# Kernel optimization log

Hardware: AMD Instinct MI355X
Metric: run time of the kernel (lower is better)

The kernel has to match this reference:

```python
import jax, jax.numpy as jnp
import numpy as np

B, N, F, L = 16, 1536, 128, 2   # batch, input_features, enc(=dec)_features, n_layers
SLOPE = 0.2                      # LeakyReLU alpha
NEG = -1e9                       # mask fill for softmax


def setup_inputs() -> dict:
    key = jax.random.key(0)
    ks = jax.random.split(key, 14)
    g = lambda k, shape, s=0.05: (jax.random.normal(k, shape, jnp.float32) * s)
    data = jax.random.randint(ks[0], (B, N), 0, 2)          # binary presence vector
    embed = g(ks[1], (N + 1, F)).at[0].set(0.0)              # padding_idx=0 row zeroed
    return {
        "data": data,
        "embed": embed,
        "enc_W": g(ks[2], (L, F, F)),
        "enc_a_src": g(ks[3], (L, F)),
        "enc_a_dst": g(ks[4], (L, F)),
        "param_W": g(ks[5], (F, 2 * F)),
        "param_b": g(ks[6], (2 * F,)),
        "dec_W": g(ks[7], (F, F)),
        "dec_a_src": g(ks[8], (F,)),
        "dec_a_dst": g(ks[9], (F,)),
        "out_W1": g(ks[10], (F, F)),
        "out_b1": g(ks[11], (F,)),
        "out_W2": g(ks[12], (F, 1)),
        "out_b2": g(ks[13], (1,)),
    }


def _gat(x, mask, W, a_src, a_dst):
    """Single-head graph attention over a dense boolean adjacency `mask`.
    Equivalent to sparse GAT over the clique edge list data_to_edges() builds
    (self-loops included). Rows with no edges output 0."""
    h = x @ W                                    # (n, F)
    si = h @ a_src                               # (n,)
    sj = h @ a_dst                               # (n,)
    e = jax.nn.leaky_relu(si[:, None] + sj[None, :], SLOPE)
    e = jnp.where(mask, e, NEG)
    attn = jax.nn.softmax(e, axis=-1) * mask.any(axis=-1)[:, None]
    return attn @ h                              # (n, F)


def reference(data, embed, enc_W, enc_a_src, enc_a_dst, param_W, param_b,
              dec_W, dec_a_src, dec_a_dst, out_W1, out_b1, out_W2, out_b2):
    def per_sample(g):
        d = g != 0                               # active feature nodes
        m_in = d[:, None] & d[None, :]           # input clique adjacency (N, N)
        x = embed[:-1]                           # node features = embedding rows (N, F)
        for l in range(L):                       # encoder layers (n_layers=2)
            x = jax.nn.elu(_gat(x, m_in, enc_W[l], enc_a_src[l], enc_a_dst[l]))
        # variational parameterization (eval mode: dropout=id, reparam -> mean)
        par = x @ param_W + param_b              # (N, 2F)
        mean, sigma = par[:, :F], par[:, F:]
        w = (g == 1).astype(mean.dtype)
        cnt = jnp.maximum(w.sum(), 1.0)
        kld = 0.5 * jnp.sum(w[:, None] * (jnp.exp(sigma) - sigma - 1.0 + mean ** 2)) / cnt
        # append master node (last embedding row) and decode over extended clique
        enc_full = jnp.concatenate([mean, embed[-1:]], axis=0)      # (N+1, F)
        d_ext = jnp.concatenate([d, jnp.ones((1,), bool)])
        m_out = d_ext[:, None] & d_ext[None, :]                     # (N+1, N+1)
        dec = jax.nn.relu(_gat(enc_full, m_out, dec_W, dec_a_src, dec_a_dst))
        return dec[-1], kld                      # master-node readout (F,)

    feats, klds = jax.vmap(per_sample)(data)     # (B, F), (B,)
    pred = jax.nn.relu(feats @ out_W1 + out_b1) @ out_W2 + out_b2   # (B, 1)
    return pred, jnp.sum(klds)
```

## Files before the change

### kernel.cpp

```cpp
#include <hip/hip_runtime.h>

#define BB 16
#define NN 1536
#define FF 128
#define SLOPE 0.2f
#define NS 2048
#define CH2 32
#define NCH2 48
#define TI 8
#define NPB (NN/8)
#define DCS 64
#define NDC 24

__global__ __launch_bounds__(1024) void k_sortpre(
    const int* __restrict__ data,
    const float* __restrict__ embed, const float* __restrict__ decW,
    const float* __restrict__ aS, const float* __restrict__ aD,
    const float* __restrict__ SJb, long sStride,
    int* __restrict__ actG, int* __restrict__ cntG,
    float* __restrict__ hN, float* __restrict__ sN,
    float* __restrict__ keyG, int* __restrict__ pjG,
    float* __restrict__ SBG, float* __restrict__ SDG)
{
  int b = blockIdx.x, t = threadIdx.x;
  if (b == BB){
    __shared__ float rs[2][2];
    if (t < FF){
      float acc = 0.f;
      for (int k=0;k<FF;++k) acc += embed[(long)NN*FF + k] * decW[k*FF + t];
      hN[t] = acc;
      float ps = acc * aS[t];
      float pd = acc * aD[t];
      #pragma unroll
      for (int o=32;o;o>>=1){ ps += __shfl_down(ps,o); pd += __shfl_down(pd,o); }
      if ((t&63)==0){ rs[0][t>>6]=ps; rs[1][t>>6]=pd; }
    }
    __syncthreads();
    if (t==0){ sN[0]=rs[0][0]+rs[0][1]; sN[1]=rs[1][0]+rs[1][1]; }
    return;
  }

  __shared__ float key[NS]; __shared__ int pj[NS];
  __shared__ float sb[NS]; __shared__ float sd[NS];
  __shared__ int cntS;
  int cnt;
  if (data != nullptr){
    __shared__ int s[256];
    const int PER = NN/256;
    int local[NN/256]; int nl = 0;
    if (t < 256){
      int base = t*PER;
      #pragma unroll
      for (int u=0; u<PER; ++u){
        if (data[b*NN + base + u] != 0) local[nl++] = base+u;
      }
      s[t]=nl;
    }
    __syncthreads();
    if (t==0){ int run=0; for (int i=0;i<256;i++){ int v=s[i]; s[i]=run; run+=v; }
               cntG[b]=run; cntS=run; }
    __syncthreads();
    if (t < 256){
      int o = s[t];
      for (int u=0; u<nl; ++u) actG[b*NN + o + u] = local[u];
    }
    __syncthreads();
    cnt = cntS;
  } else {
    cnt = cntG[b];
  }

  const float* SJ = SJb + (long)b*sStride;
  const int* act = (data != nullptr) ? actG + b*NN : nullptr;
  int NSort = 32; while (NSort < cnt) NSort <<= 1;

  for (int e=t; e<NSort; e+=1024){
    if (e<cnt){ int io = act ? act[e] : e; key[e]=SJ[io]; pj[e]=io; }
    else { key[e]=__builtin_inff(); pj[e]=0; }
  }
  __syncthreads();

  for (int k=2; k<=NSort; k<<=1){
    for (int j=k>>1; j>=64; j>>=1){
      for (int e=t; e<NSort; e+=1024){
        int l = e ^ j;
        if (l > e){
          bool asc = ((e & k) == 0);
          float a0=key[e], a1=key[l];
          if (asc ? (a0>a1) : (a0<a1)){
            key[e]=a1; key[l]=a0; int p=pj[e]; pj[e]=pj[l]; pj[l]=p;
          }
        }
      }
      __syncthreads();
    }
    {
      float v0=0.f, v1=0.f; int q0=0, q1=0;
      if (t < NSort){ v0=key[t]; q0=pj[t]; }
      if (NSort > 1024){ v1=key[t+1024]; q1=pj[t+1024]; }
      int jstart = ((k>>1) < 32) ? (k>>1) : 32;
      for (int j=jstart; j>0; j>>=1){
        {
          float ov=__shfl_xor(v0,j); int oq=__shfl_xor(q0,j);
          bool keepmin = (((t & k)==0) == ((t & j)==0));
          bool take = keepmin ? (ov < v0) : (ov > v0);
          if (take){ v0=ov; q0=oq; }
        }
        if (NSort > 1024){
          int e = t+1024;
          float ov=__shfl_xor(v1,j); int oq=__shfl_xor(q1,j);
          bool keepmin = (((e & k)==0) == ((e & j)==0));
          bool take = keepmin ? (ov < v1) : (ov > v1);
          if (take){ v1=ov; q1=oq; }
        }
      }
      if (t < NSort){ key[t]=v0; pj[t]=q0; }
      if (NSort > 1024){ key[t+1024]=v1; pj[t+1024]=q1; }
    }
    __syncthreads();
  }

  {
    int e0 = 2*t, e1 = 2*t+1;
    float b0=0.f,b1=0.f,d0=0.f,d1=0.f;
    if (e0 < cnt){ float kk=key[e0]; b0=__expf(kk); d0=__expf(SLOPE*kk); }
    if (e1 < cnt){ float kk=key[e1]; b1=__expf(kk); d1=__expf(SLOPE*kk); }
    float sB=b0+b1, sD=d0+d1;
    int lane = t & 63, wid = t >> 6;
    float iB=sB, iD=sD;
    #pragma unroll
    for (int o=1;o<64;o<<=1){
      float uB=__shfl_up(iB,o), uD=__shfl_up(iD,o);
      if (lane>=o){ iB+=uB; iD+=uD; }
    }
    __shared__ float wsB[16], wsD[16];
    if (lane==63){ wsB[wid]=iB; wsD[wid]=iD; }
    __syncthreads();
    float offB=0.f, offD=0.f;
    for (int w=0; w<wid; ++w){ offB+=wsB[w]; offD+=wsD[w]; }
    float exB = offB + iB - sB;
    float exD = offD + iD - sD;
    if (e0 < NSort){ sb[e0]=exB+b0;    sd[e0]=exD+d0; }
    if (e1 < NSort){ sb[e1]=exB+b0+b1; sd[e1]=exD+d0+d1; }
  }
  __syncthreads();

  for (int e=t; e<cnt; e+=1024){
    keyG[(long)b*NN+e]=key[e]; pjG[(long)b*NN+e]=pj[e];
    SBG[(long)b*NN+e]=sb[e];   SDG[(long)b*NN+e]=sd[e];
  }
}

__global__ __launch_bounds__(128) void k_rowmm(const float* __restrict__ Xv,
    const float* __restrict__ W, const float* __restrict__ aS, const float* __restrict__ aD,
    float* __restrict__ H, float* __restrict__ SI, float* __restrict__ SJ)
{
  int r0 = blockIdx.x*8;
  int f = threadIdx.x;
  __shared__ float xs[8][FF];
  #pragma unroll
  for (int r=0;r<8;++r) xs[r][f] = Xv[(long)(r0+r)*FF + f];
  __syncthreads();
  float acc[8]={0.f,0.f,0.f,0.f,0.f,0.f,0.f,0.f};
  for (int k=0;k<FF;++k){
    float w = W[k*FF + f];
    #pragma unroll
    for (int r=0;r<8;++r) acc[r] += xs[r][k]*w;
  }
  float as = aS[f], ad = aD[f];
  __shared__ float red[2][8][2];
  #pragma unroll
  for (int r=0;r<8;++r){
    H[(long)(r0+r)*FF + f] = acc[r];
    float ps = acc[r]*as, pd = acc[r]*ad;
    #pragma unroll
    for (int o=32;o;o>>=1){ ps += __shfl_down(ps,o); pd += __shfl_down(pd,o); }
    if ((f&63)==0){ red[0][r][f>>6]=ps; red[1][r][f>>6]=pd; }
  }
  __syncthreads();
  if (f<8){
    SI[r0+f]=red[0][f][0]+red[0][f][1]; SJ[r0+f]=red[1][f][0]+red[1][f][1];
  }
}

__global__ __launch_bounds__(128) void k_chunk(
    const float* __restrict__ keyG, const int* __restrict__ pjG,
    const int* __restrict__ cntArr,
    const float* __restrict__ Hb, long hStride,
    float* __restrict__ PP, float* __restrict__ PM)
{
  int b = blockIdx.y, c = blockIdx.x, f = threadIdx.x;
  int cnt = cntArr[b];
  int k0 = c*CH2;
  if (k0 >= cnt) return;
  int k1 = k0+CH2; if (k1 > cnt) k1 = cnt;
  int kn = k1-k0;
  const float* H = Hb + (long)b*hStride + f;
  __shared__ int pjs[CH2]; __shared__ float wbs[CH2], wds[CH2];
  if (f < CH2 && f < kn){
    float kk = keyG[(long)b*NN + k0 + f];
    pjs[f] = pjG[(long)b*NN + k0 + f];
    wbs[f] = __expf(kk);
    wds[f] = __expf(SLOPE*kk);
  }
  __syncthreads();
  float accB=0.f, accD=0.f;
  float hbuf[8];
  #pragma unroll
  for (int i=0;i<8;i++) hbuf[i] = (i<kn) ? H[(long)pjs[i]*FF] : 0.f;
  long obase = ((long)b*NN + k0)*FF + f;
  int k=0;
  for (; k+8<=kn; k+=8){
    #pragma unroll
    for (int u=0;u<8;u++){
      float hv = hbuf[u];
      int kp = k+u+8;
      hbuf[u] = (kp<kn) ? H[(long)pjs[kp]*FF] : 0.f;
      accB = fmaf(wbs[k+u], hv, accB);
      accD = fmaf(wds[k+u], hv, accD);
      PP[obase + (long)(k+u)*FF] = accB;
      PM[obase + (long)(k+u)*FF] = accD;
    }
  }
  for (; k<kn; ++k){
    float hv = H[(long)pjs[k]*FF];
    accB = fmaf(wbs[k], hv, accB);
    accD = fmaf(wds[k], hv, accD);
    PP[obase + (long)k*FF] = accB;
    PM[obase + (long)k*FF] = accD;
  }
}

__global__ __launch_bounds__(128) void k_offs(
    const float* __restrict__ PP, const float* __restrict__ PM,
    const int* __restrict__ cntArr,
    float* __restrict__ OFB, float* __restrict__ OFD)
{
  int b = blockIdx.x, f = threadIdx.x;
  int cnt = cntArr[b];
  float rb=0.f, rd=0.f;
  long base = (long)b*(NCH2+1)*FF + f;
  for (int c=0;c<NCH2;++c){
    OFB[base + (long)c*FF] = rb;
    OFD[base + (long)c*FF] = rd;
    int k0 = c*CH2;
    if (k0 < cnt){
      int kend = k0+CH2; if (kend > cnt) kend = cnt; kend -= 1;
      rb += PP[((long)b*NN+kend)*FF+f];
      rd += PM[((long)b*NN+kend)*FF+f];
    }
  }
  OFB[base + (long)NCH2*FF] = rb;
  OFD[base + (long)NCH2*FF] = rd;
}

__global__ __launch_bounds__(128) void k_aggout_mm(
    const float* __restrict__ keyG, const float* __restrict__ SBG, const float* __restrict__ SDG,
    const float* __restrict__ PP, const float* __restrict__ PM,
    const float* __restrict__ OFB, const float* __restrict__ OFD,
    const float* __restrict__ SI1, const int* __restrict__ actB,
    const int* __restrict__ cntArr,
    const float* __restrict__ W, const float* __restrict__ aS, const float* __restrict__ aD,
    float* __restrict__ Hout, float* __restrict__ SIo, float* __restrict__ SJo)
{
  int b = blockIdx.y;
  int cnt = cntArr[b];
  int r0 = blockIdx.x*TI;
  if (r0 >= cnt) return;
  int f = threadIdx.x;
  const int* act = actB + b*NN;
  __shared__ float keys[NN];
  __shared__ int kk[TI]; __shared__ float sis[TI];
  __shared__ float xs2[TI][FF];

  for (int e=f; e<cnt; e+=128) keys[e] = keyG[(long)b*NN + e];
  __syncthreads();
  if (f < TI){
    int r = r0 + f;
    float si=0.f; int k=0;
    if (r < cnt){
      si = SI1[act[r]];
      float th = -si;
      int lo=0, hi=cnt;
      while (lo<hi){ int mid=(lo+hi)>>1; if (keys[mid]<=th) lo=mid+1; else hi=mid; }
      k = lo;
    }
    kk[f]=k; sis[f]=si;
  }
  __syncthreads();
  const float* ofb = OFB + (long)b*(NCH2+1)*FF;
  const float* ofd = OFD + (long)b*(NCH2+1)*FF;
  float TB  = ofb[(long)NCH2*FF + f];
  float TBs = SBG[(long)b*NN + (cnt-1)];
  int rmax = cnt - r0; if (rmax > TI) rmax = TI;
  for (int r=0; r<TI; ++r){
    float v = 0.f;
    if (r < rmax){
      int k = kk[r]; float si = sis[r];
      float PB=0.f, PD=0.f, SBv=0.f, SDv=0.f;
      if (k > 0){
        int c = (k-1)/CH2;
        PB = PP[((long)b*NN+(k-1))*FF+f] + ofb[(long)c*FF+f];
        PD = PM[((long)b*NN+(k-1))*FF+f] + ofd[(long)c*FF+f];
        SBv = SBG[(long)b*NN+(k-1)];
        SDv = SDG[(long)b*NN+(k-1)];
      }
      float ai=__expf(si), ci=__expf(SLOPE*si);
      float num = ai*(TB -PB ) + ci*PD;
      float den = ai*(TBs-SBv) + ci*SDv;
      float o2 = num/den;
      v = (o2>0.f)? o2 : (__expf(o2)-1.f);
    }
    xs2[r][f] = v;
  }
  __syncthreads();
  float acc2[TI];
  #pragma unroll
  for (int u=0;u<TI;++u) acc2[u]=0.f;
  for (int k=0;k<FF;k+=4){
    float w0 = W[(k  )*FF + f];
    float w1 = W[(k+1)*FF + f];
    float w2 = W[(k+2)*FF + f];
    float w3 = W[(k+3)*FF + f];
    #pragma unroll
    for (int u=0;u<TI;++u){
      float4 x = *reinterpret_cast<const float4*>(&xs2[u][k]);
      acc2[u] = fmaf(x.x,w0, fmaf(x.y,w1, fmaf(x.z,w2, fmaf(x.w,w3, acc2[u]))));
    }
  }
  float as = aS[f], ad = aD[f];
  __shared__ float red[2][TI][2];
  #pragma unroll
  for (int u=0;u<TI;++u){
    int rr=r0+u;
    if (rr<cnt) Hout[((long)b*NN+rr)*FF+f] = acc2[u];
    float ps = acc2[u]*as, pd = acc2[u]*ad;
    #pragma unroll
    for (int o=32;o;o>>=1){ ps += __shfl_down(ps,o); pd += __shfl_down(pd,o); }
    if ((f&63)==0){ red[0][u][f>>6]=ps; red[1][u][f>>6]=pd; }
  }
  __syncthreads();
  if (f < TI){
    int rr=r0+f;
    if (rr<cnt){
      SIo[(long)b*NN+rr]=red[0][f][0]+red[0][f][1];
      SJo[(long)b*NN+rr]=red[1][f][0]+red[1][f][1];
    }
  }
}

__global__ __launch_bounds__(128) void k_aggout(
    const float* __restrict__ keyG, const float* __restrict__ SBG, const float* __restrict__ SDG,
    const float* __restrict__ PP, const float* __restrict__ PM,
    const float* __restrict__ OFB, const float* __restrict__ OFD,
    const float* __restrict__ SIb,
    const int* __restrict__ cntArr, float* __restrict__ XoB)
{
  int b = blockIdx.y;
  int cnt = cntArr[b];
  int r0 = blockIdx.x*TI;
  if (r0 >= cnt) return;
  int f = threadIdx.x;
  const float* SI = SIb + (long)b*NN;
  float* xo = XoB + (long)b*NN*FF;
  __shared__ float keys[NN];
  __shared__ int kk[TI]; __shared__ float sis[TI];

  for (int e=f; e<cnt; e+=128) keys[e] = keyG[(long)b*NN + e];
  __syncthreads();
  if (f < TI){
    int r = r0 + f;
    float si=0.f; int k=0;
    if (r < cnt){
      si = SI[r];
      float th = -si;
      int lo=0, hi=cnt;
      while (lo<hi){ int mid=(lo+hi)>>1; if (keys[mid]<=th) lo=mid+1; else hi=mid; }
      k = lo;
    }
    kk[f]=k; sis[f]=si;
  }
  __syncthreads();
  const float* ofb = OFB + (long)b*(NCH2+1)*FF;
  const float* ofd = OFD + (long)b*(NCH2+1)*FF;
  float TB  = ofb[(long)NCH2*FF + f];
  float TBs = SBG[(long)b*NN + (cnt-1)];
  int rmax = cnt - r0; if (rmax > TI) rmax = TI;
  for (int r=0; r<rmax; ++r){
    int k = kk[r]; float si = sis[r];
    float PB=0.f, PD=0.f, SBv=0.f, SDv=0.f;
    if (k > 0){
      int c = (k-1)/CH2;
      PB = PP[((long)b*NN+(k-1))*FF+f] + ofb[(long)c*FF+f];
      PD = PM[((long)b*NN+(k-1))*FF+f] + ofd[(long)c*FF+f];
      SBv = SBG[(long)b*NN+(k-1)];
      SDv = SDG[(long)b*NN+(k-1)];
    }
    float ai=__expf(si), ci=__expf(SLOPE*si);
    float num = ai*(TB -PB ) + ci*PD;
    float den = ai*(TBs-SBv) + ci*SDv;
    float o2 = num/den;
    xo[(long)(r0+r)*FF + f] = (o2>0.f)? o2 : (__expf(o2)-1.f);
  }
}

__global__ __launch_bounds__(256) void k_pardec(const float* __restrict__ XC,
    const float* __restrict__ pW, const float* __restrict__ pB,
    const float* __restrict__ decW, const float* __restrict__ dAd,
    float* __restrict__ KPART, float* __restrict__ H3, float* __restrict__ SJd,
    const int* __restrict__ cntArr)
{
  int b = blockIdx.y; int cnt = cntArr[b];
  int bx = blockIdx.x;
  int r0 = bx*8;
  int t = threadIdx.x;
  if (r0>=cnt){
    if (t==0) KPART[b*NPB + bx] = 0.f;
    return;
  }
  const float* X = XC + (long)b*NN*FF;
  __shared__ float xs[8][FF];
  for (int e=t; e<8*FF; e+=256){
    int r=e>>7, k=e&127; int rr=r0+r;
    xs[r][k] = (rr<cnt) ? X[(long)rr*FF+k] : 0.f;
  }
  __syncthreads();
  float acc[8]={0.f,0.f,0.f,0.f,0.f,0.f,0.f,0.f};
  for (int k=0;k<FF;++k){
    float w = pW[k*2*FF + t];
    #pragma unroll
    for (int r=0;r<8;++r) acc[r]+=xs[r][k]*w;
  }
  float bb = pB[t];
  float kacc=0.f;
  #pragma unroll
  for (int r=0;r<8;++r){
    int rr=r0+r;
    if (rr>=cnt) continue;
    float v = acc[r]+bb;
    if (t<FF) kacc += v*v;
    else kacc += __expf(v)-v-1.f;
  }
  #pragma unroll
  for (int o=32;o;o>>=1) kacc += __shfl_down(kacc,o);
  __shared__ float rw[4];
  if ((t&63)==0) rw[t>>6]=kacc;
  __syncthreads();
  if (t==0) KPART[b*NPB + bx] = rw[0]+rw[1]+rw[2]+rw[3];
  __shared__ float ms[8][FF];
  if (t < FF){
    #pragma unroll
    for (int r=0;r<8;++r){
      int rr=r0+r;
      ms[r][t] = (rr<cnt) ? acc[r]+bb : 0.f;
    }
  }
  __syncthreads();
  int h = t>>7, f = t&127;
  float a2[4]={0.f,0.f,0.f,0.f};
  for (int k=0;k<FF;++k){
    float w = decW[k*FF + f];
    #pragma unroll
    for (int u=0;u<4;++u) a2[u] += ms[h*4+u][k]*w;
  }
  float ad = dAd[f];
  __shared__ float redD[8][2];
  #pragma unroll
  for (int u=0;u<4;++u){
    int rq = h*4+u; int rr = r0+rq;
    if (rr<cnt) H3[((long)b*NN+rr)*FF+f] = a2[u];
    float pd = a2[u]*ad;
    #pragma unroll
    for (int o=32;o;o>>=1) pd += __shfl_down(pd,o);
    if ((t&63)==0) redD[rq][(t>>6)&1]=pd;
  }
  __syncthreads();
  if (t<8){
    int rr=r0+t;
    if (rr<cnt) SJd[(long)b*NN+rr]=redD[t][0]+redD[t][1];
  }
}

__global__ __launch_bounds__(128) void k_dec(const float* __restrict__ H3,
    const float* __restrict__ SJ3, const float* __restrict__ sN,
    const int* __restrict__ cntArr, float* __restrict__ DECP)
{
  int b=blockIdx.y, ch=blockIdx.x;
  int cnt=cntArr[b];
  int f=threadIdx.x;
  int r0=ch*DCS; int r1 = (r0+DCS < cnt) ? r0+DCS : cnt;
  float siN = sN[0];
  const float* H = H3 + (long)b*NN*FF;
  const float* SJ = SJ3 + (long)b*NN;
  float accV=0.f, accW=0.f;
  for (int r=r0;r<r1;++r){
    float sj=SJ[r]; float x=siN+sj;
    float e=(x>=0.f)? x : SLOPE*x;
    float w=__expf(e);
    accV += w*H[(long)r*FF+f];
    accW += w;
  }
  float* P = DECP + (long)(b*NDC+ch)*(FF+1);
  P[f]=accV;
  if (f==0) P[FF]=accW;
}

__global__ __launch_bounds__(128) void k_head(const float* __restrict__ DECP,
    const float* __restrict__ hN, const float* __restrict__ sN,
    const float* __restrict__ KPART, const int* __restrict__ cntArr,
    const float* __restrict__ W1, const float* __restrict__ b1,
    const float* __restrict__ W2, const float* __restrict__ b2,
    float* __restrict__ out)
{
  int b = blockIdx.x;
  int f = threadIdx.x;
  __shared__ float rw[2];
  if (b < BB){
    float siN=sN[0], sjN=sN[1];
    float xN=siN+sjN; float eN=(xN>=0.f)?xN:SLOPE*xN; float wN=__expf(eN);
    float num=0.f, den=0.f;
    for (int c=0;c<NDC;++c){
      const float* P = DECP + (long)(b*NDC+c)*(FF+1);
      num += P[f]; den += P[FF];
    }
    num += wN*hN[f]; den += wN;
    float v = num/den;
    __shared__ float feats[FF];
    feats[f] = (v>0.f)? v : 0.f;
    __syncthreads();
    float acc=0.f;
    for (int k=0;k<FF;++k) acc += feats[k]*W1[k*FF+f];
    acc += b1[f];
    acc = (acc>0.f)? acc : 0.f;
    float p = acc*W2[f];
    #pragma unroll
    for (int o=32;o;o>>=1) p += __shfl_down(p,o);
    if ((f&63)==0) rw[f>>6]=p;
    __syncthreads();
    if (f==0) out[b] = rw[0]+rw[1]+b2[0];
  } else {
    float s=0.f;
    for (int bb=0;bb<BB;++bb){
      float part=0.f;
      for (int c=f;c<NPB;c+=128) part += KPART[bb*NPB + c];
      #pragma unroll
      for (int o=32;o;o>>=1) part += __shfl_down(part,o);
      if ((f&63)==0) rw[f>>6]=part;
      __syncthreads();
      float tot = rw[0]+rw[1];
      int c=cntArr[bb]; float cf = (c>0)? (float)c : 1.f;
      s += 0.5f*tot/cf;
      __syncthreads();
    }
    if (f==0) out[16]=s;
  }
}

extern "C" void kernel_launch(void* const* d_in, const int* in_sizes, int n_in,
                              void* d_out, int out_size, void* d_ws, size_t ws_size,
                              hipStream_t stream)
{
  const int*   data  = (const int*)d_in[0];
  const float* embed = (const float*)d_in[1];
  const float* encW  = (const float*)d_in[2];
  const float* encAs = (const float*)d_in[3];
  const float* encAd = (const float*)d_in[4];
  const float* pW    = (const float*)d_in[5];
  const float* pB    = (const float*)d_in[6];
  const float* decW  = (const float*)d_in[7];
  const float* decAs = (const float*)d_in[8];
  const float* decAd = (const float*)d_in[9];
  const float* oW1   = (const float*)d_in[10];
  const float* oB1   = (const float*)d_in[11];
  const float* oW2   = (const float*)d_in[12];
  const float* oB2   = (const float*)d_in[13];
  float* out = (float*)d_out;

  float* w = (float*)d_ws;
  long o = 0;
  float* H1   = w+o; o += (long)NN*FF;
  float* H2   = w+o; o += (long)BB*NN*FF;
  float* XC   = w+o; o += (long)BB*NN*FF;
  float* PP   = w+o; o += (long)BB*NN*FF;
  float* PM   = w+o; o += (long)BB*NN*FF;
  float* SI1  = w+o; o += NN;
  float* SJ1  = w+o; o += NN;
  float* SI2  = w+o; o += (long)BB*NN;
  float* SJ2  = w+o; o += (long)BB*NN;
  float* KPART= w+o; o += (long)BB*NPB;
  float* hN   = w+o; o += FF;
  float* sN   = w+o; o += 2;
  float* DECP = w+o; o += (long)BB*NDC*(FF+1);
  float* keyG = w+o; o += (long)BB*NN;
  float* SBG  = w+o; o += (long)BB*NN;
  float* SDG  = w+o; o += (long)BB*NN;
  float* OFB  = w+o; o += (long)BB*(NCH2+1)*FF;
  float* OFD  = w+o; o += (long)BB*(NCH2+1)*FF;
  int* act = (int*)(w+o); o += (long)BB*NN;
  int* pjG = (int*)(w+o); o += (long)BB*NN;
  int* cnt = (int*)(w+o); o += BB;
  (void)in_sizes; (void)n_in; (void)out_size; (void)ws_size;

  k_rowmm<<<NN/8,128,0,stream>>>(embed, encW, encAs, encAd, H1, SI1, SJ1);
  k_sortpre<<<BB+1,1024,0,stream>>>(data, embed, decW, decAs, decAd,
      SJ1, 0L, act, cnt, hN, sN, keyG, pjG, SBG, SDG);
  k_chunk<<<dim3(NCH2,BB),128,0,stream>>>(keyG, pjG, cnt, H1, 0L, PP, PM);
  k_offs<<<BB,128,0,stream>>>(PP, PM, cnt, OFB, OFD);
  k_aggout_mm<<<dim3(NN/TI,BB),128,0,stream>>>(keyG, SBG, SDG, PP, PM, OFB, OFD,
      SI1, act, cnt, encW + FF*FF, encAs + FF, encAd + FF, H2, SI2, SJ2);
  k_sortpre<<<BB,1024,0,stream>>>(nullptr, embed, decW, decAs, decAd,
      SJ2, (long)NN, act, cnt, hN, sN, keyG, pjG, SBG, SDG);
  k_chunk<<<dim3(NCH2,BB),128,0,stream>>>(keyG, pjG, cnt, H2, (long)NN*FF, PP, PM);
  k_offs<<<BB,128,0,stream>>>(PP, PM, cnt, OFB, OFD);
  k_aggout<<<dim3(NN/TI,BB),128,0,stream>>>(keyG, SBG, SDG, PP, PM, OFB, OFD,
      SI2, cnt, XC);
  k_pardec<<<dim3(NPB,BB),256,0,stream>>>(XC, pW, pB, decW, decAd,
      KPART, H2 , SJ2 , cnt);
  k_dec<<<dim3(NDC,BB),128,0,stream>>>(H2 , SJ2, sN, cnt, DECP);
  k_head<<<BB+1,128,0,stream>>>(DECP, hN, sN, KPART, cnt, oW1, oB1, oW2, oB2, out);
}
```

Baseline: 263.4 us.

## Precompute per-row softmax params in sort kernel, parallelize offsets, shrink chunks

Moves the per-row binary search, exponentials and denominator computation out of the aggregation kernels into the sort kernel. The sort kernel writes one float4 per row, so each aggregation block no longer reloads the whole key array into shared memory and searches it. The early bitonic stages now run entirely in registers with shuffles. The offset prefix kernel is parallelized over 4 groups with 512 threads, and chunk and decoder split sizes are halved to expose more blocks. Aggregation loads are hoisted into unrolled batches to raise memory-level parallelism. The cost is extra serial work inside the 16-block sort kernel and more chunk launches.

```diff
diff --git a/kernel.cpp b/kernel.cpp
--- a/kernel.cpp
+++ b/kernel.cpp
@@ -5,22 +5,25 @@
 #define FF 128
 #define SLOPE 0.2f
 #define NS 2048
-#define CH2 32
-#define NCH2 48
+#define CH2 16
+#define NCH2 96
 #define TI 8
 #define NPB (NN/8)
-#define DCS 64
-#define NDC 24
+#define DCS 32
+#define NDC 48
+#define OG 4
+#define OC (NCH2/OG)
 
 __global__ __launch_bounds__(1024) void k_sortpre(
     const int* __restrict__ data,
     const float* __restrict__ embed, const float* __restrict__ decW,
     const float* __restrict__ aS, const float* __restrict__ aD,
     const float* __restrict__ SJb, long sStride,
+    const float* __restrict__ SIr, long siStride,
     int* __restrict__ actG, int* __restrict__ cntG,
     float* __restrict__ hN, float* __restrict__ sN,
     float* __restrict__ keyG, int* __restrict__ pjG,
-    float* __restrict__ SBG, float* __restrict__ SDG)
+    float* __restrict__ ROWP)
 {
   int b = blockIdx.x, t = threadIdx.x;
   if (b == BB){
@@ -80,7 +83,36 @@
   }
   __syncthreads();
 
-  for (int k=2; k<=NSort; k<<=1){
+  {
+    float v0 = (t<NSort)? key[t] : __builtin_inff();
+    int   q0 = (t<NSort)? pj[t] : 0;
+    float v1 = __builtin_inff(); int q1 = 0;
+    bool two = (NSort > 1024);
+    if (two){ v1=key[t+1024]; q1=pj[t+1024]; }
+    int kmax = (NSort < 64)? NSort : 64;
+    for (int k=2; k<=kmax; k<<=1){
+      for (int j=k>>1; j>0; j>>=1){
+        {
+          float ov=__shfl_xor(v0,j); int oq=__shfl_xor(q0,j);
+          bool keepmin = (((t & k)==0) == ((t & j)==0));
+          bool take = keepmin ? (ov < v0) : (ov > v0);
+          if (take){ v0=ov; q0=oq; }
+        }
+        if (two){
+          int e = t+1024;
+          float ov=__shfl_xor(v1,j); int oq=__shfl_xor(q1,j);
+          bool keepmin = (((e & k)==0) == ((e & j)==0));
+          bool take = keepmin ? (ov < v1) : (ov > v1);
+          if (take){ v1=ov; q1=oq; }
+        }
+      }
+    }
+    if (t < NSort){ key[t]=v0; pj[t]=q0; }
+    if (two){ key[t+1024]=v1; pj[t+1024]=q1; }
+  }
+  __syncthreads();
+
+  for (int k=128; k<=NSort; k<<=1){
     for (int j=k>>1; j>=64; j>>=1){
       for (int e=t; e<NSort; e+=1024){
         int l = e ^ j;
@@ -98,8 +130,7 @@
       float v0=0.f, v1=0.f; int q0=0, q1=0;
       if (t < NSort){ v0=key[t]; q0=pj[t]; }
       if (NSort > 1024){ v1=key[t+1024]; q1=pj[t+1024]; }
-      int jstart = ((k>>1) < 32) ? (k>>1) : 32;
-      for (int j=jstart; j>0; j>>=1){
+      for (int j=32; j>0; j>>=1){
         {
           float ov=__shfl_xor(v0,j); int oq=__shfl_xor(q0,j);
           bool keepmin = (((t & k)==0) == ((t & j)==0));
@@ -145,9 +176,22 @@
   }
   __syncthreads();
 
-  for (int e=t; e<cnt; e+=1024){
-    keyG[(long)b*NN+e]=key[e]; pjG[(long)b*NN+e]=pj[e];
-    SBG[(long)b*NN+e]=sb[e];   SDG[(long)b*NN+e]=sd[e];
+  {
+    float TBs = sb[(cnt>0)? cnt-1 : 0];
+    const float* SIrb = SIr + (data ? 0L : (long)b*siStride);
+    for (int r=t; r<cnt; r+=1024){
+      float si = data ? SIrb[act[r]] : SIrb[r];
+      float th = -si;
+      int lo=0, hi=cnt;
+      while (lo<hi){ int mid=(lo+hi)>>1; if (key[mid]<=th) lo=mid+1; else hi=mid; }
+      float ai=__expf(si), ci=__expf(SLOPE*si);
+      float SBv = (lo>0)? sb[lo-1] : 0.f;
+      float SDv = (lo>0)? sd[lo-1] : 0.f;
+      float4 rp;
+      rp.x=ai; rp.y=ci; rp.z = ai*(TBs-SBv)+ci*SDv; rp.w=__int_as_float(lo);
+      reinterpret_cast<float4*>(ROWP)[(long)b*NN+r] = rp;
+      keyG[(long)b*NN+r]=key[r]; pjG[(long)b*NN+r]=pj[r];
+    }
   }
 }
 
@@ -231,34 +275,53 @@
   }
 }
 
-__global__ __launch_bounds__(128) void k_offs(
+__global__ __launch_bounds__(512) void k_offs(
     const float* __restrict__ PP, const float* __restrict__ PM,
     const int* __restrict__ cntArr,
     float* __restrict__ OFB, float* __restrict__ OFD)
 {
-  int b = blockIdx.x, f = threadIdx.x;
+  int b = blockIdx.x; int t = threadIdx.x;
+  int f = t & 127, g = t >> 7;
   int cnt = cntArr[b];
+  float vB[OC], vD[OC];
+  #pragma unroll
+  for (int i=0;i<OC;++i){
+    int c = g*OC + i; int k0 = c*CH2;
+    int ke = k0+CH2; if (ke>cnt) ke=cnt; ke-=1; if (ke<0) ke=0;
+    float pb = PP[((long)b*NN+ke)*FF+f];
+    float pm = PM[((long)b*NN+ke)*FF+f];
+    bool on = (k0 < cnt);
+    vB[i] = on? pb : 0.f; vD[i] = on? pm : 0.f;
+  }
   float rb=0.f, rd=0.f;
+  #pragma unroll
+  for (int i=0;i<OC;++i){
+    float tb=vB[i], td=vD[i];
+    vB[i]=rb; vD[i]=rd;
+    rb+=tb; rd+=td;
+  }
+  __shared__ float totB[OG][128], totD[OG][128];
+  totB[g][f]=rb; totD[g][f]=rd;
+  __syncthreads();
+  float ob=0.f, od=0.f;
+  #pragma unroll
+  for (int q=0;q<OG;++q){ if (q<g){ ob+=totB[q][f]; od+=totD[q][f]; } }
   long base = (long)b*(NCH2+1)*FF + f;
-  for (int c=0;c<NCH2;++c){
-    OFB[base + (long)c*FF] = rb;
-    OFD[base + (long)c*FF] = rd;
-    int k0 = c*CH2;
-    if (k0 < cnt){
-      int kend = k0+CH2; if (kend > cnt) kend = cnt; kend -= 1;
-      rb += PP[((long)b*NN+kend)*FF+f];
-      rd += PM[((long)b*NN+kend)*FF+f];
-    }
-  }
-  OFB[base + (long)NCH2*FF] = rb;
-  OFD[base + (long)NCH2*FF] = rd;
+  #pragma unroll
+  for (int i=0;i<OC;++i){
+    OFB[base + (long)(g*OC+i)*FF] = ob + vB[i];
+    OFD[base + (long)(g*OC+i)*FF] = od + vD[i];
+  }
+  if (g == OG-1){
+    OFB[base + (long)NCH2*FF] = ob + rb;
+    OFD[base + (long)NCH2*FF] = od + rd;
+  }
 }
 
 __global__ __launch_bounds__(128) void k_aggout_mm(
-    const float* __restrict__ keyG, const float* __restrict__ SBG, const float* __restrict__ SDG,
     const float* __restrict__ PP, const float* __restrict__ PM,
     const float* __restrict__ OFB, const float* __restrict__ OFD,
-    const float* __restrict__ SI1, const int* __restrict__ actB,
+    const float* __restrict__ ROWP,
     const int* __restrict__ cntArr,
     const float* __restrict__ W, const float* __restrict__ aS, const float* __restrict__ aD,
     float* __restrict__ Hout, float* __restrict__ SIo, float* __restrict__ SJo)
@@ -268,50 +331,42 @@
   int r0 = blockIdx.x*TI;
   if (r0 >= cnt) return;
   int f = threadIdx.x;
-  const int* act = actB + b*NN;
-  __shared__ float keys[NN];
-  __shared__ int kk[TI]; __shared__ float sis[TI];
+  __shared__ float4 srow[TI];
   __shared__ float xs2[TI][FF];
-
-  for (int e=f; e<cnt; e+=128) keys[e] = keyG[(long)b*NN + e];
-  __syncthreads();
   if (f < TI){
-    int r = r0 + f;
-    float si=0.f; int k=0;
-    if (r < cnt){
-      si = SI1[act[r]];
-      float th = -si;
-      int lo=0, hi=cnt;
-      while (lo<hi){ int mid=(lo+hi)>>1; if (keys[mid]<=th) lo=mid+1; else hi=mid; }
-      k = lo;
-    }
-    kk[f]=k; sis[f]=si;
+    int r = r0+f; if (r > cnt-1) r = cnt-1;
+    srow[f] = reinterpret_cast<const float4*>(ROWP)[(long)b*NN + r];
   }
   __syncthreads();
   const float* ofb = OFB + (long)b*(NCH2+1)*FF;
   const float* ofd = OFD + (long)b*(NCH2+1)*FF;
-  float TB  = ofb[(long)NCH2*FF + f];
-  float TBs = SBG[(long)b*NN + (cnt-1)];
+  float TB = ofb[(long)NCH2*FF + f];
   int rmax = cnt - r0; if (rmax > TI) rmax = TI;
-  for (int r=0; r<TI; ++r){
+  float pb[TI], pd[TI], ob[TI], od[TI];
+  #pragma unroll
+  for (int u=0;u<TI;++u){
+    int k = __float_as_int(srow[u].w);
+    int kc = k-1; if (kc < 0) kc = 0;
+    int c = kc/CH2;
+    pb[u] = PP[((long)b*NN+kc)*FF+f];
+    pd[u] = PM[((long)b*NN+kc)*FF+f];
+    ob[u] = ofb[(long)c*FF+f];
+    od[u] = ofd[(long)c*FF+f];
+  }
+  #pragma unroll
+  for (int u=0;u<TI;++u){
+    float4 rp = srow[u];
+    int k = __float_as_int(rp.w);
+    bool hasP = (k > 0);
+    float PB = hasP ? (pb[u]+ob[u]) : 0.f;
+    float PD = hasP ? (pd[u]+od[u]) : 0.f;
+    float num = rp.x*(TB-PB) + rp.y*PD;
     float v = 0.f;
-    if (r < rmax){
-      int k = kk[r]; float si = sis[r];
-      float PB=0.f, PD=0.f, SBv=0.f, SDv=0.f;
-      if (k > 0){
-        int c = (k-1)/CH2;
-        PB = PP[((long)b*NN+(k-1))*FF+f] + ofb[(long)c*FF+f];
-        PD = PM[((long)b*NN+(k-1))*FF+f] + ofd[(long)c*FF+f];
-        SBv = SBG[(long)b*NN+(k-1)];
-        SDv = SDG[(long)b*NN+(k-1)];
-      }
-      float ai=__expf(si), ci=__expf(SLOPE*si);
-      float num = ai*(TB -PB ) + ci*PD;
-      float den = ai*(TBs-SBv) + ci*SDv;
-      float o2 = num/den;
+    if (u < rmax){
+      float o2 = num/rp.z;
       v = (o2>0.f)? o2 : (__expf(o2)-1.f);
     }
-    xs2[r][f] = v;
+    xs2[u][f] = v;
   }
   __syncthreads();
   float acc2[TI];
@@ -334,10 +389,10 @@
   for (int u=0;u<TI;++u){
     int rr=r0+u;
     if (rr<cnt) Hout[((long)b*NN+rr)*FF+f] = acc2[u];
-    float ps = acc2[u]*as, pd = acc2[u]*ad;
-    #pragma unroll
-    for (int o=32;o;o>>=1){ ps += __shfl_down(ps,o); pd += __shfl_down(pd,o); }
-    if ((f&63)==0){ red[0][u][f>>6]=ps; red[1][u][f>>6]=pd; }
+    float ps = acc2[u]*as, pd2 = acc2[u]*ad;
+    #pragma unroll
+    for (int o=32;o;o>>=1){ ps += __shfl_down(ps,o); pd2 += __shfl_down(pd2,o); }
+    if ((f&63)==0){ red[0][u][f>>6]=ps; red[1][u][f>>6]=pd2; }
   }
   __syncthreads();
   if (f < TI){
@@ -350,10 +405,9 @@
 }
 
 __global__ __launch_bounds__(128) void k_aggout(
-    const float* __restrict__ keyG, const float* __restrict__ SBG, const float* __restrict__ SDG,
     const float* __restrict__ PP, const float* __restrict__ PM,
     const float* __restrict__ OFB, const float* __restrict__ OFD,
-    const float* __restrict__ SIb,
+    const float* __restrict__ ROWP,
     const int* __restrict__ cntArr, float* __restrict__ XoB)
 {
   int b = blockIdx.y;
@@ -361,46 +415,40 @@
   int r0 = blockIdx.x*TI;
   if (r0 >= cnt) return;
   int f = threadIdx.x;
-  const float* SI = SIb + (long)b*NN;
   float* xo = XoB + (long)b*NN*FF;
-  __shared__ float keys[NN];
-  __shared__ int kk[TI]; __shared__ float sis[TI];
-
-  for (int e=f; e<cnt; e+=128) keys[e] = keyG[(long)b*NN + e];
-  __syncthreads();
+  __shared__ float4 srow[TI];
   if (f < TI){
-    int r = r0 + f;
-    float si=0.f; int k=0;
-    if (r < cnt){
-      si = SI[r];
-      float th = -si;
-      int lo=0, hi=cnt;
-      while (lo<hi){ int mid=(lo+hi)>>1; if (keys[mid]<=th) lo=mid+1; else hi=mid; }
-      k = lo;
-    }
-    kk[f]=k; sis[f]=si;
+    int r = r0+f; if (r > cnt-1) r = cnt-1;
+    srow[f] = reinterpret_cast<const float4*>(ROWP)[(long)b*NN + r];
   }
   __syncthreads();
   const float* ofb = OFB + (long)b*(NCH2+1)*FF;
   const float* ofd = OFD + (long)b*(NCH2+1)*FF;
-  float TB  = ofb[(long)NCH2*FF + f];
-  float TBs = SBG[(long)b*NN + (cnt-1)];
+  float TB = ofb[(long)NCH2*FF + f];
   int rmax = cnt - r0; if (rmax > TI) rmax = TI;
-  for (int r=0; r<rmax; ++r){
-    int k = kk[r]; float si = sis[r];
-    float PB=0.f, PD=0.f, SBv=0.f, SDv=0.f;
-    if (k > 0){
-      int c = (k-1)/CH2;
-      PB = PP[((long)b*NN+(k-1))*FF+f] + ofb[(long)c*FF+f];
-      PD = PM[((long)b*NN+(k-1))*FF+f] + ofd[(long)c*FF+f];
-      SBv = SBG[(long)b*NN+(k-1)];
-      SDv = SDG[(long)b*NN+(k-1)];
-    }
-    float ai=__expf(si), ci=__expf(SLOPE*si);
-    float num = ai*(TB -PB ) + ci*PD;
-    float den = ai*(TBs-SBv) + ci*SDv;
-    float o2 = num/den;
-    xo[(long)(r0+r)*FF + f] = (o2>0.f)? o2 : (__expf(o2)-1.f);
+  float pb[TI], pd[TI], ob[TI], od[TI];
+  #pragma unroll
+  for (int u=0;u<TI;++u){
+    int k = __float_as_int(srow[u].w);
+    int kc = k-1; if (kc < 0) kc = 0;
+    int c = kc/CH2;
+    pb[u] = PP[((long)b*NN+kc)*FF+f];
+    pd[u] = PM[((long)b*NN+kc)*FF+f];
+    ob[u] = ofb[(long)c*FF+f];
+    od[u] = ofd[(long)c*FF+f];
+  }
+  #pragma unroll
+  for (int u=0;u<TI;++u){
+    if (u < rmax){
+      float4 rp = srow[u];
+      int k = __float_as_int(rp.w);
+      bool hasP = (k > 0);
+      float PB = hasP ? (pb[u]+ob[u]) : 0.f;
+      float PD = hasP ? (pd[u]+od[u]) : 0.f;
+      float num = rp.x*(TB-PB) + rp.y*PD;
+      float o2 = num/rp.z;
+      xo[(long)(r0+u)*FF + f] = (o2>0.f)? o2 : (__expf(o2)-1.f);
+    }
   }
 }
 
@@ -592,10 +640,10 @@
   float* sN   = w+o; o += 2;
   float* DECP = w+o; o += (long)BB*NDC*(FF+1);
   float* keyG = w+o; o += (long)BB*NN;
-  float* SBG  = w+o; o += (long)BB*NN;
-  float* SDG  = w+o; o += (long)BB*NN;
   float* OFB  = w+o; o += (long)BB*(NCH2+1)*FF;
   float* OFD  = w+o; o += (long)BB*(NCH2+1)*FF;
+  o = (o+3) & ~3L;
+  float* ROWP = w+o; o += (long)BB*NN*4;
   int* act = (int*)(w+o); o += (long)BB*NN;
   int* pjG = (int*)(w+o); o += (long)BB*NN;
   int* cnt = (int*)(w+o); o += BB;
@@ -603,17 +651,16 @@
 
   k_rowmm<<<NN/8,128,0,stream>>>(embed, encW, encAs, encAd, H1, SI1, SJ1);
   k_sortpre<<<BB+1,1024,0,stream>>>(data, embed, decW, decAs, decAd,
-      SJ1, 0L, act, cnt, hN, sN, keyG, pjG, SBG, SDG);
+      SJ1, 0L, SI1, 0L, act, cnt, hN, sN, keyG, pjG, ROWP);
   k_chunk<<<dim3(NCH2,BB),128,0,stream>>>(keyG, pjG, cnt, H1, 0L, PP, PM);
-  k_offs<<<BB,128,0,stream>>>(PP, PM, cnt, OFB, OFD);
-  k_aggout_mm<<<dim3(NN/TI,BB),128,0,stream>>>(keyG, SBG, SDG, PP, PM, OFB, OFD,
-      SI1, act, cnt, encW + FF*FF, encAs + FF, encAd + FF, H2, SI2, SJ2);
+  k_offs<<<BB,512,0,stream>>>(PP, PM, cnt, OFB, OFD);
+  k_aggout_mm<<<dim3(NN/TI,BB),128,0,stream>>>(PP, PM, OFB, OFD, ROWP,
+      cnt, encW + FF*FF, encAs + FF, encAd + FF, H2, SI2, SJ2);
   k_sortpre<<<BB,1024,0,stream>>>(nullptr, embed, decW, decAs, decAd,
-      SJ2, (long)NN, act, cnt, hN, sN, keyG, pjG, SBG, SDG);
+      SJ2, (long)NN, SI2, (long)NN, act, cnt, hN, sN, keyG, pjG, ROWP);
   k_chunk<<<dim3(NCH2,BB),128,0,stream>>>(keyG, pjG, cnt, H2, (long)NN*FF, PP, PM);
-  k_offs<<<BB,128,0,stream>>>(PP, PM, cnt, OFB, OFD);
-  k_aggout<<<dim3(NN/TI,BB),128,0,stream>>>(keyG, SBG, SDG, PP, PM, OFB, OFD,
-      SI2, cnt, XC);
+  k_offs<<<BB,512,0,stream>>>(PP, PM, cnt, OFB, OFD);
+  k_aggout<<<dim3(NN/TI,BB),128,0,stream>>>(PP, PM, OFB, OFD, ROWP, cnt, XC);
   k_pardec<<<dim3(NPB,BB),256,0,stream>>>(XC, pW, pB, decW, decAd,
       KPART, H2 , SJ2 , cnt);
   k_dec<<<dim3(NDC,BB),128,0,stream>>>(H2 , SJ2, sN, cnt, DECP);
```

Result: faster. 239.1 us (-9.2%).
